# Performance work log

Hardware: AMD Instinct MI355X
Metric: run time of the kernel (lower is better)

The kernel has to match this reference:

```python
import jax, jax.numpy as jnp
import numpy as np

N = 8192        # nodes
E = 131072      # edges (avg degree 16)
IN_DIM = 6      # x_end - x_start
HID = 256
OUT = 256
N_EXP = 8
N_LAYERS = 3
TOP_K = 2
N_GRAPHS = 64


def setup_inputs() -> dict:
    key = jax.random.key(0)
    ks = jax.random.split(key, 12)
    def lin(k, fan_in, shape):
        return jax.random.normal(k, shape, jnp.float32) * (1.0 / np.sqrt(fan_in))
    x = jax.random.normal(ks[0], (N, IN_DIM), jnp.float32)
    edge_index = jax.random.randint(ks[1], (2, E), 0, N)
    batch = jnp.sort(jax.random.randint(ks[2], (N,), 0, N_GRAPHS))
    return {
        "x": x,
        "edge_index": edge_index,
        "batch": batch,
        "enc_W": lin(ks[3], IN_DIM, (IN_DIM, HID)),
        "enc_b": jnp.zeros((HID,), jnp.float32),
        "q_W": lin(ks[4], HID + 2, (HID + 2, HID)),
        "q_b": jnp.zeros((HID,), jnp.float32),
        "k_W": lin(ks[5], HID + 2, (HID + 2, HID)),
        "k_b": jnp.zeros((HID,), jnp.float32),
        "v_W": lin(ks[6], HID + 2, (HID + 2, HID)),
        "v_b": jnp.zeros((HID,), jnp.float32),
        "out_W": lin(ks[7], HID, (HID, N_EXP)),
        "out_b": jnp.zeros((N_EXP,), jnp.float32),
        "exp_Wh": lin(ks[8], HID, (N_EXP, N_LAYERS - 1, HID, HID)),
        "exp_bh": jnp.zeros((N_EXP, N_LAYERS - 1, HID), jnp.float32),
        "exp_Wo": lin(ks[9], HID, (N_EXP, HID, OUT)),
        "exp_bo": jnp.zeros((N_EXP, OUT), jnp.float32),
    }


def reference(x, edge_index, batch, enc_W, enc_b, q_W, q_b, k_W, k_b,
              v_W, v_b, out_W, out_b, exp_Wh, exp_bh, exp_Wo, exp_bo):
    # --- shared encoder ---
    h = jax.nn.relu(x @ enc_W + enc_b)                     # [N, HID]

    # --- per-graph size features broadcast back to nodes ---
    src, dst = edge_index[0], edge_index[1]
    ones_n = jnp.ones((N,), h.dtype)
    ones_e = jnp.ones((E,), h.dtype)
    nodes_per_g = jax.ops.segment_sum(ones_n, batch, num_segments=N_GRAPHS)
    edges_per_g = jax.ops.segment_sum(ones_e, batch[src], num_segments=N_GRAPHS)
    size_feat = jnp.stack([jnp.log1p(nodes_per_g)[batch],
                           jnp.log1p(edges_per_g)[batch]], axis=-1)  # [N, 2]

    z = jnp.concatenate([h, size_feat], axis=-1)           # [N, HID+2]

    # --- dense self-attention router ---
    q = z @ q_W + q_b
    k = z @ k_W + k_b
    v = z @ v_W + v_b
    scale = 1.0 / np.sqrt(z.shape[-1])
    attn = jax.nn.softmax((q @ k.T) * scale, axis=-1)      # [N, N]
    fused = attn @ v                                       # [N, HID]
    logits = fused @ out_W + out_b                         # [N, N_EXP]

    # --- sparse top-k routing (renormalized top-k of softmax probs) ---
    probs = jax.nn.softmax(logits, axis=-1)
    top_v, top_i = jax.lax.top_k(probs, TOP_K)
    rows = jnp.arange(N)[:, None]
    sparse = jnp.zeros_like(probs).at[rows, top_i].set(top_v)
    sparse = sparse / sparse.sum(axis=-1, keepdims=True)   # [N, N_EXP]

    # --- experts: stacked graph-conv towers (vectorized over experts) ---
    deg = jnp.clip(jax.ops.segment_sum(ones_e, dst, num_segments=N), 1.0, None)
    def neigh_mean(He):  # He: [N_EXP, N, d]
        agg = jax.vmap(lambda he: jax.ops.segment_sum(he[src], dst, num_segments=N))(He)
        return agg / deg[None, :, None]

    He = jnp.broadcast_to(h[None], (N_EXP, N, HID))
    for l in range(N_LAYERS - 1):
        He = jax.nn.relu(
            jnp.einsum('enh,ehk->enk', He + neigh_mean(He), exp_Wh[:, l])
            + exp_bh[:, l][:, None, :])
    Y = jnp.einsum('enh,eho->eno', He + neigh_mean(He), exp_Wo) + exp_bo[:, None, :]

    # --- top-k dense-masked combine: (y * sparse[...,None]).sum(expert dim) ---
    return jnp.einsum('eno,ne->no', Y, sparse)             # [N, OUT]
```

## Files before the change

### kernel.cpp

```cpp
#include <hip/hip_runtime.h>
#include <math.h>

#define NN 8192
#define NE 131072
#define ZK 288
#define NG 64
#define ASPLIT 16
#define QB 256
#define KB 32

typedef __attribute__((ext_vector_type(8))) short bf16x8;
typedef __attribute__((ext_vector_type(4))) float f32x4;
typedef __attribute__((ext_vector_type(8))) _Float16 f16x8;
typedef __attribute__((ext_vector_type(4))) _Float16 f16x4;

static __device__ __forceinline__ unsigned short f2bf(float f) {
    unsigned u = __float_as_uint(f);
    unsigned r = (u + 0x7FFFu + ((u >> 16) & 1u)) >> 16;
    return (unsigned short)r;
}
static __device__ __forceinline__ float b2f(unsigned short h) {
    return __uint_as_float(((unsigned)h) << 16);
}

__global__ __launch_bounds__(256) void k_counts(const int* __restrict__ ei,
    const int* __restrict__ batch, int* ncnt, int* ecnt, int* indeg)
{
    __shared__ int he[NG], hn[NG];
    const int t = threadIdx.x, b = blockIdx.x;
    if (t < NG) { he[t] = 0; hn[t] = 0; }
    __syncthreads();
    const int e0 = b * (NE / 64);
#pragma unroll
    for (int i = 0; i < (NE / 64) / 256; ++i) {
        int idx = e0 + i * 256 + t;
        int src = ei[idx], dst = ei[NE + idx];
        atomicAdd(&he[batch[src]], 1);
        atomicAdd(&indeg[dst], 1);
    }
    if (t < 128) atomicAdd(&hn[batch[b * 128 + t]], 1);
    __syncthreads();
    if (t < NG) {
        if (he[t]) atomicAdd(&ecnt[t], he[t]);
        if (hn[t]) atomicAdd(&ncnt[t], hn[t]);
    }
}

__global__ __launch_bounds__(256) void k_encoder(const float* __restrict__ x,
    const float* __restrict__ encW, const float* __restrict__ encb,
    const int* __restrict__ batch, const int* __restrict__ ncnt,
    const int* __restrict__ ecnt, float* __restrict__ z,
    unsigned short* __restrict__ zb)
{
    int n = blockIdx.x, c = threadIdx.x;
    __shared__ float xr[8];
    if (c < 6) xr[c] = x[n * 6 + c];
    __syncthreads();
    float a = encb[c];
#pragma unroll
    for (int i = 0; i < 6; ++i) a = fmaf(xr[i], encW[i * 256 + c], a);
    float h = fmaxf(a, 0.f);
    z[n * ZK + c] = h;
    zb[n * 256 + c] = f2bf(h);
    if (c == 0) {
        int g = batch[n];
        z[n * ZK + 256] = log1pf((float)ncnt[g]);
        z[n * ZK + 257] = log1pf((float)ecnt[g]);
    }
    if (c >= 2 && c < 32) z[n * ZK + 256 + c] = 0.f;
}

__global__ __launch_bounds__(256) void k_scan(const int* __restrict__ indeg,
                                              int* __restrict__ rowptr)
{
    __shared__ int part[256];
    int t = threadIdx.x;
    int base = t * 32, s = 0;
    for (int i = 0; i < 32; ++i) s += indeg[base + i];
    part[t] = s;
    __syncthreads();
    if (t == 0) {
        int run = 0;
        for (int i = 0; i < 256; ++i) { int v = part[i]; part[i] = run; run += v; }
        rowptr[NN] = run;
    }
    __syncthreads();
    int run = part[t];
    for (int i = 0; i < 32; ++i) { rowptr[base + i] = run; run += indeg[base + i]; }
}

__global__ __launch_bounds__(256) void k_fill(const int* __restrict__ ei,
    const int* __restrict__ rowptr, int* __restrict__ cursor, int* __restrict__ colidx)
{
    int tid = blockIdx.x * 256 + threadIdx.x;
    if (tid >= NE) return;
    int dst = ei[NE + tid];
    int pos = atomicAdd(&cursor[dst], 1);
    colidx[rowptr[dst] + pos] = ei[tid];
}

__global__ __launch_bounds__(256) void k_prep_qk(const float* __restrict__ qW,
    const float* __restrict__ kW, float* __restrict__ Wq, float* __restrict__ Wk)
{
    int idx = blockIdx.x * 256 + threadIdx.x;
    int r = idx >> 8, c = idx & 255;
    Wq[idx] = (r < 258) ? qW[r * 256 + c] : 0.f;
    Wk[idx] = (r < 258) ? kW[r * 256 + c] : 0.f;
}

__global__ __launch_bounds__(256) void k_prep_vo(const float* __restrict__ vW,
    const float* __restrict__ vb, const float* __restrict__ outW,
    float* __restrict__ Wvo, float* __restrict__ bvo)
{
    int idx = blockIdx.x * 256 + threadIdx.x;
    if (idx < ZK * 8) {
        int r = idx >> 3, e = idx & 7;
        float s = 0.f;
        if (r < 258)
            for (int c = 0; c < 256; ++c) s = fmaf(vW[r * 256 + c], outW[c * 8 + e], s);
        Wvo[idx] = s;
    } else if (idx < ZK * 8 + 8) {
        int e = idx - ZK * 8;
        float s = 0.f;
        for (int c = 0; c < 256; ++c) s = fmaf(vb[c], outW[c * 8 + e], s);
        bvo[e] = s;
    }
}

__global__ __launch_bounds__(256) void k_prep_w(const float* __restrict__ eWh,
    const float* __restrict__ eWo, unsigned short* __restrict__ Bth,
    unsigned short* __restrict__ Bto)
{
    int id = blockIdx.x * 256 + threadIdx.x;
    if (id < 16 * 65536) {
        int h = id & 255, kcol = (id >> 8) & 255, m = id >> 16;
        Bth[id] = f2bf(eWh[((size_t)m * 256 + h) * 256 + kcol]);
    } else if (id < 24 * 65536) {
        int j = id - 16 * 65536;
        int h = j & 255, o = (j >> 8) & 255, e = j >> 16;
        Bto[j] = f2bf(eWo[((size_t)e * 256 + h) * 256 + o]);
    }
}

__global__ __launch_bounds__(256) void k_gemm_qk(
    const float* __restrict__ A,
    const float* __restrict__ Wq, const float* __restrict__ Wk,
    const float* __restrict__ qb, const float* __restrict__ kb,
    _Float16* __restrict__ qh, _Float16* __restrict__ ql,
    _Float16* __restrict__ kh, _Float16* __restrict__ kl,
    float scale, int K)
{
    const float* B    = blockIdx.z ? Wk : Wq;
    const float* bias = blockIdx.z ? kb : qb;
    _Float16* Ch = blockIdx.z ? kh : qh;
    _Float16* Cl = blockIdx.z ? kl : ql;
    const float scl = blockIdx.z ? 1.0f : scale;
    __shared__ float As[32][132];
    __shared__ float Bs[32][68];
    int t = threadIdx.x;
    int m0 = blockIdx.y * 128, n0 = blockIdx.x * 64;
    int tr = t & 15, tc = t >> 4;
    float acc[8][4];
#pragma unroll
    for (int i = 0; i < 8; ++i)
#pragma unroll
        for (int j = 0; j < 4; ++j) acc[i][j] = 0.f;

    for (int k0 = 0; k0 < K; k0 += 32) {
#pragma unroll
        for (int i = 0; i < 4; ++i) {
            int f = t + 256 * i;
            int kc = f & 7, row = f >> 3;
            float4 v = *(const float4*)&A[(size_t)(m0 + row) * ZK + k0 + 4 * kc];
            As[4 * kc + 0][row] = v.x; As[4 * kc + 1][row] = v.y;
            As[4 * kc + 2][row] = v.z; As[4 * kc + 3][row] = v.w;
        }
#pragma unroll
        for (int i = 0; i < 2; ++i) {
            int f = t + 256 * i;
            int nc = f & 15, krow = f >> 4;
            *(float4*)&Bs[krow][4 * nc] =
                *(const float4*)&B[(size_t)(k0 + krow) * 256 + n0 + 4 * nc];
        }
        __syncthreads();
#pragma unroll
        for (int kk = 0; kk < 32; ++kk) {
            float4 a0 = *(const float4*)&As[kk][4 * tr];
            float4 a1 = *(const float4*)&As[kk][64 + 4 * tr];
            float4 b  = *(const float4*)&Bs[kk][4 * tc];
            const float av0[4] = {a0.x, a0.y, a0.z, a0.w};
            const float av1[4] = {a1.x, a1.y, a1.z, a1.w};
            const float bv[4]  = {b.x, b.y, b.z, b.w};
#pragma unroll
            for (int i = 0; i < 4; ++i)
#pragma unroll
                for (int j = 0; j < 4; ++j) {
                    acc[i][j]     = fmaf(av0[i], bv[j], acc[i][j]);
                    acc[4 + i][j] = fmaf(av1[i], bv[j], acc[4 + i][j]);
                }
        }
        __syncthreads();
    }
    float4 bi = *(const float4*)&bias[n0 + 4 * tc];
    const float bb[4] = {bi.x, bi.y, bi.z, bi.w};
#pragma unroll
    for (int h = 0; h < 2; ++h)
#pragma unroll
        for (int i = 0; i < 4; ++i) {
            int m = m0 + h * 64 + 4 * tr + i;
            f16x4 vh, vl;
#pragma unroll
            for (int j = 0; j < 4; ++j) {
                float v = (acc[h * 4 + i][j] + bb[j]) * scl;
                _Float16 hi = (_Float16)v;
                vh[j] = hi;
                vl[j] = (_Float16)(v - (float)hi);
            }
            *(f16x4*)&Ch[(size_t)m * 256 + n0 + 4 * tc] = vh;
            *(f16x4*)&Cl[(size_t)m * 256 + n0 + 4 * tc] = vl;
        }
}

__global__ __launch_bounds__(512) void k_gemm_bf(
    const unsigned short* __restrict__ A,
    const unsigned short* __restrict__ Bt,
    const float* __restrict__ bias,
    unsigned short* __restrict__ Cb,
    float* __restrict__ Ys,
    const float* __restrict__ sparse,
    const int* __restrict__ i1,
    long long aStrideZ, long long btStrideZ, long long cStrideZ, int biasStrideZ,
    int mode)
{
    const int bid = blockIdx.x;
    const int ez = bid & 7;
    const int tile = bid >> 3;
    const int n0 = (tile & 1) * 128, m0 = (tile >> 1) * 128;
    A    += (size_t)ez * aStrideZ;
    Bt   += (size_t)ez * btStrideZ;
    bias += (size_t)ez * biasStrideZ;
    if (mode == 0) Cb += (size_t)ez * cStrideZ;
    __shared__ unsigned short As[128][40];
    __shared__ unsigned short Bs[128][40];
    const int t = threadIdx.x;
    const int wid = t >> 6, lane = t & 63;
    const int wr = wid >> 2, wc = wid & 3;
    const int lr = lane & 15, lg = lane >> 4;
    f32x4 acc[4][2];
#pragma unroll
    for (int mf = 0; mf < 4; ++mf)
#pragma unroll
        for (int nf = 0; nf < 2; ++nf) acc[mf][nf] = (f32x4){0.f, 0.f, 0.f, 0.f};

    const int rA = t >> 2, cA = t & 3;
    for (int k0 = 0; k0 < 256; k0 += 32) {
        uint4 va = *(const uint4*)&A[(size_t)(m0 + rA) * 256 + k0 + 8 * cA];
        uint4 vB = *(const uint4*)&Bt[(size_t)(n0 + rA) * 256 + k0 + 8 * cA];
        *(uint4*)&As[rA][8 * cA] = va;
        *(uint4*)&Bs[rA][8 * cA] = vB;
        __syncthreads();
        bf16x8 a[4], b[2];
#pragma unroll
        for (int mf = 0; mf < 4; ++mf)
            a[mf] = *(const bf16x8*)&As[wr * 64 + mf * 16 + lr][8 * lg];
#pragma unroll
        for (int nf = 0; nf < 2; ++nf)
            b[nf] = *(const bf16x8*)&Bs[wc * 32 + nf * 16 + lr][8 * lg];
#pragma unroll
        for (int mf = 0; mf < 4; ++mf)
#pragma unroll
            for (int nf = 0; nf < 2; ++nf)
                acc[mf][nf] = __builtin_amdgcn_mfma_f32_16x16x32_bf16(
                    a[mf], b[nf], acc[mf][nf], 0, 0, 0);
        __syncthreads();
    }
    if (mode == 0) {
#pragma unroll
        for (int mf = 0; mf < 4; ++mf)
#pragma unroll
            for (int reg = 0; reg < 4; ++reg) {
                int m = m0 + wr * 64 + mf * 16 + lg * 4 + reg;
#pragma unroll
                for (int nf = 0; nf < 2; ++nf) {
                    int c = n0 + wc * 32 + nf * 16 + lr;
                    float v = acc[mf][nf][reg] + bias[c];
                    Cb[(size_t)m * 256 + c] = f2bf(fmaxf(v, 0.f));
                }
            }
    } else {
#pragma unroll
        for (int mf = 0; mf < 4; ++mf)
#pragma unroll
            for (int reg = 0; reg < 4; ++reg) {
                int m = m0 + wr * 64 + mf * 16 + lg * 4 + reg;
                float w = sparse[m * 8 + ez];
                if (w != 0.f) {
                    int slot = (ez == i1[m]) ? 0 : 1;
                    float* dst = Ys + (size_t)slot * NN * 256 + (size_t)m * 256;
#pragma unroll
                    for (int nf = 0; nf < 2; ++nf) {
                        int c = n0 + wc * 32 + nf * 16 + lr;
                        dst[c] = w * (acc[mf][nf][reg] + bias[c]);
                    }
                }
            }
    }
}

__global__ __launch_bounds__(256) void k_vo(const float* __restrict__ z,
    const float* __restrict__ Wvo, const float* __restrict__ bvo,
    float* __restrict__ vo)
{
    int n = blockIdx.x * 4 + (threadIdx.x >> 6);
    int lane = threadIdx.x & 63;
    float p[8];
#pragma unroll
    for (int e = 0; e < 8; ++e) p[e] = 0.f;
    for (int kk = lane; kk < ZK; kk += 64) {
        float zv = z[(size_t)n * ZK + kk];
        float4 w0 = *(const float4*)&Wvo[kk * 8];
        float4 w1 = *(const float4*)&Wvo[kk * 8 + 4];
        p[0] = fmaf(zv, w0.x, p[0]); p[1] = fmaf(zv, w0.y, p[1]);
        p[2] = fmaf(zv, w0.z, p[2]); p[3] = fmaf(zv, w0.w, p[3]);
        p[4] = fmaf(zv, w1.x, p[4]); p[5] = fmaf(zv, w1.y, p[5]);
        p[6] = fmaf(zv, w1.z, p[6]); p[7] = fmaf(zv, w1.w, p[7]);
    }
#pragma unroll
    for (int msk = 1; msk <= 32; msk <<= 1)
#pragma unroll
        for (int e = 0; e < 8; ++e) p[e] += __shfl_xor(p[e], msk);
    if (lane == 0) {
#pragma unroll
        for (int e = 0; e < 8; ++e) vo[n * 8 + e] = p[e] + bvo[e];
    }
}

__global__ __launch_bounds__(512, 2) void k_attn_mfma(
    const _Float16* __restrict__ qh_, const _Float16* __restrict__ ql_,
    const _Float16* __restrict__ kh, const _Float16* __restrict__ kl,
    const float* __restrict__ vo, float* __restrict__ pm,
    float* __restrict__ pl, float* __restrict__ pacc)
{
    __shared__ uint4 lds[2][KB * 64];
    const int bid = blockIdx.x;
    const int split = bid & 15;
    const int rowblk = bid >> 4;
    const int n0 = rowblk * QB;
    const int t = threadIdx.x, w = t >> 6, lane = t & 63;
    const int g = lane >> 4, c = lane & 15;

    f16x8 bqh[2][8], bql[2][8];
#pragma unroll
    for (int rs = 0; rs < 2; ++rs) {
        const int row = n0 + w * 32 + rs * 16 + c;
#pragma unroll
        for (int st = 0; st < 8; ++st) {
            bqh[rs][st] = *(const f16x8*)&qh_[(size_t)row * 256 + st * 32 + g * 8];
            bql[rs][st] = *(const f16x8*)&ql_[(size_t)row * 256 + st * 32 + g * 8];
        }
    }
    float m_[2] = {-INFINITY, -INFINITY};
    float l_[2] = {0.f, 0.f};
    float pv[2][8];
#pragma unroll
    for (int rs = 0; rs < 2; ++rs)
#pragma unroll
        for (int e = 0; e < 8; ++e) pv[rs][e] = 0.f;

    const int kbase0 = split * (NN / ASPLIT);
    auto STAGE = [&](int buf, int kb) {
#pragma unroll
        for (int i = 0; i < 4; ++i) {
            int u = i * 512 + t;
            int key = u >> 6;
            int half = (u >> 5) & 1;
            int c16 = (u & 31) ^ (key & 7);
            const _Float16* src = half ? kl : kh;
            const _Float16* gp = src + (size_t)(kb + key) * 256 + c16 * 8;
            uint4* lp = &lds[buf][i * 512 + (t & ~63)];
            __builtin_amdgcn_global_load_lds(
                (const __attribute__((address_space(1))) void*)gp,
                (__attribute__((address_space(3))) void*)lp, 16, 0, 0);
        }
    };
    STAGE(0, kbase0);
    __syncthreads();
    int cur = 0;
    const int NCH = (NN / ASPLIT) / KB;
    for (int ch = 0; ch < NCH; ++ch) {
        const int kbase = kbase0 + ch * KB;
        if (ch + 1 < NCH) STAGE(cur ^ 1, kbase + KB);
#pragma unroll
        for (int kt = 0; kt < 2; ++kt) {
            const char* kbp = (const char*)lds[cur] + (kt * 16 + c) * 1024;
            const int swz = ((kt * 16 + c) & 7) << 4;
            f32x4 acc0 = (f32x4){0.f, 0.f, 0.f, 0.f};
            f32x4 acc1 = (f32x4){0.f, 0.f, 0.f, 0.f};
#pragma unroll
            for (int st = 0; st < 8; ++st) {
                const int off = (st * 64 + g * 16) ^ swz;
                f16x8 kah = *(const f16x8*)(kbp + off);
                f16x8 kal = *(const f16x8*)(kbp + 512 + off);
                acc0 = __builtin_amdgcn_mfma_f32_16x16x32_f16(kah, bqh[0][st], acc0, 0, 0, 0);
                acc0 = __builtin_amdgcn_mfma_f32_16x16x32_f16(kal, bqh[0][st], acc0, 0, 0, 0);
                acc0 = __builtin_amdgcn_mfma_f32_16x16x32_f16(kah, bql[0][st], acc0, 0, 0, 0);
                acc1 = __builtin_amdgcn_mfma_f32_16x16x32_f16(kah, bqh[1][st], acc1, 0, 0, 0);
                acc1 = __builtin_amdgcn_mfma_f32_16x16x32_f16(kal, bqh[1][st], acc1, 0, 0, 0);
                acc1 = __builtin_amdgcn_mfma_f32_16x16x32_f16(kah, bql[1][st], acc1, 0, 0, 0);
            }
            const int kb2 = kbase + kt * 16 + 4 * g;
            float4 w0[4], w1[4];
#pragma unroll
            for (int r = 0; r < 4; ++r) {
                w0[r] = *(const float4*)&vo[(kb2 + r) * 8];
                w1[r] = *(const float4*)&vo[(kb2 + r) * 8 + 4];
            }
#pragma unroll
            for (int rs = 0; rs < 2; ++rs) {
                f32x4 s = rs ? acc1 : acc0;
                float cm = fmaxf(fmaxf(s[0], s[1]), fmaxf(s[2], s[3]));
                float mn = fmaxf(m_[rs], cm);
                float rsc = __expf(m_[rs] - mn);
                float p0 = __expf(s[0] - mn);
                float p1 = __expf(s[1] - mn);
                float p2 = __expf(s[2] - mn);
                float p3 = __expf(s[3] - mn);
                l_[rs] = l_[rs] * rsc + (p0 + p1 + p2 + p3);
                m_[rs] = mn;
                pv[rs][0] = pv[rs][0]*rsc + p0*w0[0].x + p1*w0[1].x + p2*w0[2].x + p3*w0[3].x;
                pv[rs][1] = pv[rs][1]*rsc + p0*w0[0].y + p1*w0[1].y + p2*w0[2].y + p3*w0[3].y;
                pv[rs][2] = pv[rs][2]*rsc + p0*w0[0].z + p1*w0[1].z + p2*w0[2].z + p3*w0[3].z;
                pv[rs][3] = pv[rs][3]*rsc + p0*w0[0].w + p1*w0[1].w + p2*w0[2].w + p3*w0[3].w;
                pv[rs][4] = pv[rs][4]*rsc + p0*w1[0].x + p1*w1[1].x + p2*w1[2].x + p3*w1[3].x;
                pv[rs][5] = pv[rs][5]*rsc + p0*w1[0].y + p1*w1[1].y + p2*w1[2].y + p3*w1[3].y;
                pv[rs][6] = pv[rs][6]*rsc + p0*w1[0].z + p1*w1[1].z + p2*w1[2].z + p3*w1[3].z;
                pv[rs][7] = pv[rs][7]*rsc + p0*w1[0].w + p1*w1[1].w + p2*w1[2].w + p3*w1[3].w;
            }
        }
        __syncthreads();
        cur ^= 1;
    }
#pragma unroll
    for (int msk = 16; msk <= 32; msk <<= 1) {
#pragma unroll
        for (int rs = 0; rs < 2; ++rs) {
            float mo = __shfl_xor(m_[rs], msk);
            float lo = __shfl_xor(l_[rs], msk);
            float mn = fmaxf(m_[rs], mo);
            float a = __expf(m_[rs] - mn), b = __expf(mo - mn);
            l_[rs] = l_[rs] * a + lo * b;
#pragma unroll
            for (int e = 0; e < 8; ++e) {
                float po = __shfl_xor(pv[rs][e], msk);
                pv[rs][e] = pv[rs][e] * a + po * b;
            }
            m_[rs] = mn;
        }
    }
    if (g == 0) {
#pragma unroll
        for (int rs = 0; rs < 2; ++rs) {
            int n = n0 + w * 32 + rs * 16 + c;
            pm[split * NN + n] = m_[rs];
            pl[split * NN + n] = l_[rs];
#pragma unroll
            for (int e = 0; e < 8; ++e)
                pacc[(size_t)split * NN * 8 + n * 8 + e] = pv[rs][e];
        }
    }
}

__global__ __launch_bounds__(256) void k_attn_merge(
    const float* __restrict__ pm, const float* __restrict__ pl,
    const float* __restrict__ pacc, const float* __restrict__ outb,
    float* __restrict__ sparse, int* __restrict__ i1o)
{
    int n = blockIdx.x * 256 + threadIdx.x;
    float mn = -INFINITY;
#pragma unroll
    for (int s = 0; s < ASPLIT; ++s) mn = fmaxf(mn, pm[s * NN + n]);
    float l = 0.f;
    float lg[8];
#pragma unroll
    for (int e = 0; e < 8; ++e) lg[e] = 0.f;
#pragma unroll
    for (int s = 0; s < ASPLIT; ++s) {
        float r = __expf(pm[s * NN + n] - mn);
        l += pl[s * NN + n] * r;
#pragma unroll
        for (int e = 0; e < 8; ++e)
            lg[e] += pacc[(size_t)s * NN * 8 + n * 8 + e] * r;
    }
    float inv = 1.f / l;
#pragma unroll
    for (int e = 0; e < 8; ++e) lg[e] = lg[e] * inv + outb[e];
    int i1 = 0; float v1 = lg[0];
#pragma unroll
    for (int e = 1; e < 8; ++e) if (lg[e] > v1) { v1 = lg[e]; i1 = e; }
    int i2 = -1; float v2 = -INFINITY;
#pragma unroll
    for (int e = 0; e < 8; ++e) if (e != i1 && lg[e] > v2) { v2 = lg[e]; i2 = e; }
    float e2 = __expf(v2 - v1);
    float w1 = 1.f / (1.f + e2);
    float w2 = e2 / (1.f + e2);
#pragma unroll
    for (int e = 0; e < 8; ++e)
        sparse[n * 8 + e] = (e == i1) ? w1 : ((e == i2) ? w2 : 0.f);
    i1o[n] = i1;
}

__global__ __launch_bounds__(256) void k_agg_b2b(
    const unsigned short* __restrict__ HeAll, const int* __restrict__ rowptr,
    const int* __restrict__ colidx, unsigned short* __restrict__ XAll,
    int eshift)
{
    const int bid = blockIdx.x;
    const int e = bid & ((1 << eshift) - 1);
    const int nb = bid >> eshift;
    const unsigned short* He = HeAll + (size_t)e * NN * 256;
    unsigned short* X = XAll + (size_t)e * NN * 256;
    int n = nb * 4 + (threadIdx.x >> 6);
    int c4 = (threadIdx.x & 63) * 4;
    int r0 = rowptr[n], r1 = rowptr[n + 1];
    float a0 = 0.f, a1 = 0.f, a2 = 0.f, a3 = 0.f;
    float b0 = 0.f, b1 = 0.f, b2 = 0.f, b3 = 0.f;
    float e0 = 0.f, e1 = 0.f, e2 = 0.f, e3 = 0.f;
    float d0 = 0.f, d1 = 0.f, d2 = 0.f, d3 = 0.f;
    int i = r0;
    for (; i + 4 <= r1; i += 4) {
        int s0 = colidx[i], s1 = colidx[i + 1], s2 = colidx[i + 2], s3 = colidx[i + 3];
        ushort4 v0 = *(const ushort4*)&He[(size_t)s0 * 256 + c4];
        ushort4 v1 = *(const ushort4*)&He[(size_t)s1 * 256 + c4];
        ushort4 v2 = *(const ushort4*)&He[(size_t)s2 * 256 + c4];
        ushort4 v3 = *(const ushort4*)&He[(size_t)s3 * 256 + c4];
        a0 += b2f(v0.x); a1 += b2f(v0.y); a2 += b2f(v0.z); a3 += b2f(v0.w);
        b0 += b2f(v1.x); b1 += b2f(v1.y); b2 += b2f(v1.z); b3 += b2f(v1.w);
        e0 += b2f(v2.x); e1 += b2f(v2.y); e2 += b2f(v2.z); e3 += b2f(v2.w);
        d0 += b2f(v3.x); d1 += b2f(v3.y); d2 += b2f(v3.z); d3 += b2f(v3.w);
    }
    for (; i < r1; ++i) {
        int sn = colidx[i];
        ushort4 v = *(const ushort4*)&He[(size_t)sn * 256 + c4];
        a0 += b2f(v.x); a1 += b2f(v.y); a2 += b2f(v.z); a3 += b2f(v.w);
    }
    a0 += b0 + e0 + d0; a1 += b1 + e1 + d1;
    a2 += b2 + e2 + d2; a3 += b3 + e3 + d3;
    int deg = r1 - r0;
    float inv = 1.f / (float)(deg > 1 ? deg : 1);
    ushort4 self = *(const ushort4*)&He[(size_t)n * 256 + c4];
    ushort4 o;
    o.x = f2bf(b2f(self.x) + a0 * inv); o.y = f2bf(b2f(self.y) + a1 * inv);
    o.z = f2bf(b2f(self.z) + a2 * inv); o.w = f2bf(b2f(self.w) + a3 * inv);
    *(ushort4*)&X[(size_t)n * 256 + c4] = o;
}

__global__ __launch_bounds__(256) void k_combine2(const float* __restrict__ Ys,
                                                  float* __restrict__ out)
{
    int i = (blockIdx.x * 256 + threadIdx.x) * 4;
    float4 a = *(const float4*)&Ys[i];
    float4 b = *(const float4*)&Ys[(size_t)NN * 256 + i];
    float4 o;
    o.x = a.x + b.x; o.y = a.y + b.y; o.z = a.z + b.z; o.w = a.w + b.w;
    *(float4*)&out[i] = o;
}

extern "C" void kernel_launch(void* const* d_in, const int* in_sizes, int n_in,
                              void* d_out, int out_size, void* d_ws, size_t ws_size,
                              hipStream_t stream)
{
    (void)n_in; (void)out_size;
    const float* x     = (const float*)d_in[0];
    const int*   ei    = (const int*)d_in[1];
    const int*   batch = (const int*)d_in[2];
    const float* encW  = (const float*)d_in[3];
    const float* encb  = (const float*)d_in[4];
    const float* qW    = (const float*)d_in[5];
    const float* qb    = (const float*)d_in[6];
    const float* kW    = (const float*)d_in[7];
    const float* kb    = (const float*)d_in[8];
    const float* vW    = (const float*)d_in[9];
    const float* vb    = (const float*)d_in[10];
    const float* outW  = (const float*)d_in[11];
    const float* outb  = (const float*)d_in[12];
    const float* eWh   = (const float*)d_in[13];
    const float* ebh   = (const float*)d_in[14];
    const float* eWo   = (const float*)d_in[15];
    const float* ebo   = (const float*)d_in[16];
    float* out = (float*)d_out;
    if (in_sizes[0] != NN * 6 || in_sizes[1] != 2 * NE) return;

    char* wsp = (char*)d_ws;
    size_t off = 0;
    auto alloc = [&](size_t bytes) -> void* {
        void* p = wsp + off;
        off += (bytes + 511) & ~(size_t)511;
        return p;
    };
    float* z   = (float*)alloc((size_t)NN * ZK * 4);
    unsigned short* zb = (unsigned short*)alloc((size_t)NN * 256 * 2);
    _Float16* qh = (_Float16*)alloc((size_t)4 * NN * 256 * 2);
    _Float16* ql = qh + (size_t)NN * 256;
    _Float16* kh = ql + (size_t)NN * 256;
    _Float16* kl = kh + (size_t)NN * 256;
    float* Ys = (float*)qh;
    float* vo     = (float*)alloc((size_t)NN * 8 * 4);
    float* sparse = (float*)alloc((size_t)NN * 8 * 4);
    int*   i1buf  = (int*)alloc((size_t)NN * 4);
    unsigned short* Xball = (unsigned short*)alloc((size_t)8 * NN * 256 * 2);
    unsigned short* Heb   = (unsigned short*)alloc((size_t)8 * NN * 256 * 2);
    unsigned short* Bth   = (unsigned short*)alloc((size_t)16 * 65536 * 2);
    unsigned short* Bto   = (unsigned short*)alloc((size_t)8 * 65536 * 2);
    float* Wq   = (float*)alloc((size_t)ZK * 256 * 4);
    float* Wk   = (float*)alloc((size_t)ZK * 256 * 4);
    float* Wvo  = (float*)alloc((size_t)ZK * 8 * 4);
    float* bvo  = (float*)alloc(8 * 4);
    float* pm   = (float*)alloc((size_t)ASPLIT * NN * 4);
    float* plb  = (float*)alloc((size_t)ASPLIT * NN * 4);
    float* pacc = (float*)alloc((size_t)ASPLIT * NN * 8 * 4);
    int* ints   = (int*)alloc((size_t)(NG + NG + NN + NN) * 4);
    int* ncnt = ints, *ecnt = ints + NG, *indeg = ecnt + NG, *cursor = indeg + NN;
    int* rowptr = (int*)alloc((size_t)(NN + 1) * 4);
    int* colidx = (int*)alloc((size_t)NE * 4);
    if (off > ws_size) return;

    hipMemsetAsync(ints, 0, (size_t)(NG + NG + NN + NN) * 4, stream);
    k_counts<<<64, 256, 0, stream>>>(ei, batch, ncnt, ecnt, indeg);
    k_prep_qk<<<ZK, 256, 0, stream>>>(qW, kW, Wq, Wk);
    k_prep_vo<<<(ZK * 8 + 8 + 255) / 256, 256, 0, stream>>>(vW, vb, outW, Wvo, bvo);
    k_prep_w<<<(24 * 65536) / 256, 256, 0, stream>>>(eWh, eWo, Bth, Bto);
    k_encoder<<<NN, 256, 0, stream>>>(x, encW, encb, batch, ncnt, ecnt, z, zb);
    k_scan<<<1, 256, 0, stream>>>(indeg, rowptr);
    k_fill<<<(NE + 255) / 256, 256, 0, stream>>>(ei, rowptr, cursor, colidx);

    float scale = 1.f / sqrtf(258.f);
    dim3 gqk(256 / 64, NN / 128, 2);
    k_gemm_qk<<<gqk, 256, 0, stream>>>(z, Wq, Wk, qb, kb, qh, ql, kh, kl, scale, ZK);
    k_vo<<<NN / 4, 256, 0, stream>>>(z, Wvo, bvo, vo);

    k_attn_mfma<<<(NN / QB) * ASPLIT, 512, 0, stream>>>(qh, ql, kh, kl, vo, pm, plb, pacc);
    k_attn_merge<<<NN / 256, 256, 0, stream>>>(pm, plb, pacc, outb, sparse, i1buf);

    k_agg_b2b<<<NN / 4, 256, 0, stream>>>(zb, rowptr, colidx, Xball, 0);
    k_gemm_bf<<<1024, 512, 0, stream>>>(Xball, Bth, ebh, Heb, nullptr, nullptr, nullptr,
                                        0, (long long)2 * 65536, (long long)NN * 256,
                                        2 * 256, 0);
    k_agg_b2b<<<(NN / 4) * 8, 256, 0, stream>>>(Heb, rowptr, colidx, Xball, 3);
    k_gemm_bf<<<1024, 512, 0, stream>>>(Xball, Bth + 65536, ebh + 256, Heb,
                                        nullptr, nullptr, nullptr,
                                        (long long)NN * 256, (long long)2 * 65536,
                                        (long long)NN * 256, 2 * 256, 0);
    k_agg_b2b<<<(NN / 4) * 8, 256, 0, stream>>>(Heb, rowptr, colidx, Xball, 3);
    k_gemm_bf<<<1024, 512, 0, stream>>>(Xball, Bto, ebo, nullptr, Ys, sparse, i1buf,
                                        (long long)NN * 256, (long long)65536,
                                        0, 256, 1);
    k_combine2<<<(NN * 256 / 4) / 256, 256, 0, stream>>>(Ys, out);
}
```

Baseline: 398.3 us.

## Compact final expert layer to routed rows only and prioritize attention MFMA

Result: slower. 410.7 us (+3.1%).

```diff
diff --git a/kernel.cpp b/kernel.cpp
--- a/kernel.cpp
+++ b/kernel.cpp
@@ -229,6 +229,8 @@
     float* __restrict__ Ys,
     const float* __restrict__ sparse,
     const int* __restrict__ i1,
+    const int* __restrict__ rowlist,
+    const int* __restrict__ rcnt,
     long long aStrideZ, long long btStrideZ, long long cStrideZ, int biasStrideZ,
     int mode)
 {
@@ -236,6 +238,8 @@
     const int ez = bid & 7;
     const int tile = bid >> 3;
     const int n0 = (tile & 1) * 128, m0 = (tile >> 1) * 128;
+    const int cnt = (mode == 1) ? rcnt[ez] : 0;
+    if (mode == 1 && m0 >= cnt) return;
     A    += (size_t)ez * aStrideZ;
     Bt   += (size_t)ez * btStrideZ;
     bias += (size_t)ez * biasStrideZ;
@@ -293,14 +297,17 @@
 #pragma unroll
             for (int reg = 0; reg < 4; ++reg) {
                 int m = m0 + wr * 64 + mf * 16 + lg * 4 + reg;
-                float w = sparse[m * 8 + ez];
-                if (w != 0.f) {
-                    int slot = (ez == i1[m]) ? 0 : 1;
-                    float* dst = Ys + (size_t)slot * NN * 256 + (size_t)m * 256;
-#pragma unroll
-                    for (int nf = 0; nf < 2; ++nf) {
-                        int c = n0 + wc * 32 + nf * 16 + lr;
-                        dst[c] = w * (acc[mf][nf][reg] + bias[c]);
+                if (m < cnt) {
+                    int n = rowlist[ez * NN + m];
+                    float w = sparse[n * 8 + ez];
+                    if (w != 0.f) {
+                        int slot = (ez == i1[n]) ? 0 : 1;
+                        float* dst = Ys + (size_t)slot * NN * 256 + (size_t)n * 256;
+#pragma unroll
+                        for (int nf = 0; nf < 2; ++nf) {
+                            int c = n0 + wc * 32 + nf * 16 + lr;
+                            dst[c] = w * (acc[mf][nf][reg] + bias[c]);
+                        }
                     }
                 }
             }
@@ -396,6 +403,7 @@
             const int swz = ((kt * 16 + c) & 7) << 4;
             f32x4 acc0 = (f32x4){0.f, 0.f, 0.f, 0.f};
             f32x4 acc1 = (f32x4){0.f, 0.f, 0.f, 0.f};
+            __builtin_amdgcn_s_setprio(1);
 #pragma unroll
             for (int st = 0; st < 8; ++st) {
                 const int off = (st * 64 + g * 16) ^ swz;
@@ -408,6 +416,7 @@
                 acc1 = __builtin_amdgcn_mfma_f32_16x16x32_f16(kal, bqh[1][st], acc1, 0, 0, 0);
                 acc1 = __builtin_amdgcn_mfma_f32_16x16x32_f16(kah, bql[1][st], acc1, 0, 0, 0);
             }
+            __builtin_amdgcn_s_setprio(0);
             const int kb2 = kbase + kt * 16 + 4 * g;
             float4 w0[4], w1[4];
 #pragma unroll
@@ -507,6 +516,31 @@
     for (int e = 0; e < 8; ++e)
         sparse[n * 8 + e] = (e == i1) ? w1 : ((e == i2) ? w2 : 0.f);
     i1o[n] = i1;
+}
+
+__global__ __launch_bounds__(256) void k_rows(const float* __restrict__ sparse,
+    int* __restrict__ rcnt, int* __restrict__ rowlist)
+{
+    __shared__ int lcnt[8], lbase[8];
+    const int t = threadIdx.x;
+    const int n = blockIdx.x * 256 + t;
+    if (t < 8) lcnt[t] = 0;
+    __syncthreads();
+    int myexp[2], myslot[2];
+    int cnt = 0;
+#pragma unroll
+    for (int e = 0; e < 8; ++e) {
+        if (sparse[n * 8 + e] != 0.f && cnt < 2) {
+            myexp[cnt] = e;
+            myslot[cnt] = atomicAdd(&lcnt[e], 1);
+            ++cnt;
+        }
+    }
+    __syncthreads();
+    if (t < 8) lbase[t] = atomicAdd(&rcnt[t], lcnt[t]);
+    __syncthreads();
+    for (int j = 0; j < cnt; ++j)
+        rowlist[myexp[j] * NN + lbase[myexp[j]] + myslot[j]] = n;
 }
 
 __global__ __launch_bounds__(256) void k_agg_b2b(
@@ -554,6 +588,55 @@
     *(ushort4*)&X[(size_t)n * 256 + c4] = o;
 }
 
+__global__ __launch_bounds__(256) void k_agg_rows(
+    const unsigned short* __restrict__ HeAll, const int* __restrict__ rowptr,
+    const int* __restrict__ colidx, const int* __restrict__ rowlist,
+    const int* __restrict__ rcnt, unsigned short* __restrict__ XAll)
+{
+    const int bid = blockIdx.x;
+    const int e = bid & 7;
+    const int nb = bid >> 3;
+    const int cnt = rcnt[e];
+    const int r = nb * 4 + (threadIdx.x >> 6);
+    if (nb * 4 >= cnt) return;
+    if (r >= cnt) return;
+    const unsigned short* He = HeAll + (size_t)e * NN * 256;
+    unsigned short* X = XAll + (size_t)e * NN * 256;
+    const int n = rowlist[e * NN + r];
+    int c4 = (threadIdx.x & 63) * 4;
+    int r0 = rowptr[n], r1 = rowptr[n + 1];
+    float a0 = 0.f, a1 = 0.f, a2 = 0.f, a3 = 0.f;
+    float b0 = 0.f, b1 = 0.f, b2 = 0.f, b3 = 0.f;
+    float e0 = 0.f, e1 = 0.f, e2 = 0.f, e3 = 0.f;
+    float d0 = 0.f, d1 = 0.f, d2 = 0.f, d3 = 0.f;
+    int i = r0;
+    for (; i + 4 <= r1; i += 4) {
+        int s0 = colidx[i], s1 = colidx[i + 1], s2 = colidx[i + 2], s3 = colidx[i + 3];
+        ushort4 v0 = *(const ushort4*)&He[(size_t)s0 * 256 + c4];
+        ushort4 v1 = *(const ushort4*)&He[(size_t)s1 * 256 + c4];
+        ushort4 v2 = *(const ushort4*)&He[(size_t)s2 * 256 + c4];
+        ushort4 v3 = *(const ushort4*)&He[(size_t)s3 * 256 + c4];
+        a0 += b2f(v0.x); a1 += b2f(v0.y); a2 += b2f(v0.z); a3 += b2f(v0.w);
+        b0 += b2f(v1.x); b1 += b2f(v1.y); b2 += b2f(v1.z); b3 += b2f(v1.w);
+        e0 += b2f(v2.x); e1 += b2f(v2.y); e2 += b2f(v2.z); e3 += b2f(v2.w);
+        d0 += b2f(v3.x); d1 += b2f(v3.y); d2 += b2f(v3.z); d3 += b2f(v3.w);
+    }
+    for (; i < r1; ++i) {
+        int sn = colidx[i];
+        ushort4 v = *(const ushort4*)&He[(size_t)sn * 256 + c4];
+        a0 += b2f(v.x); a1 += b2f(v.y); a2 += b2f(v.z); a3 += b2f(v.w);
+    }
+    a0 += b0 + e0 + d0; a1 += b1 + e1 + d1;
+    a2 += b2 + e2 + d2; a3 += b3 + e3 + d3;
+    int deg = r1 - r0;
+    float inv = 1.f / (float)(deg > 1 ? deg : 1);
+    ushort4 self = *(const ushort4*)&He[(size_t)n * 256 + c4];
+    ushort4 o;
+    o.x = f2bf(b2f(self.x) + a0 * inv); o.y = f2bf(b2f(self.y) + a1 * inv);
+    o.z = f2bf(b2f(self.z) + a2 * inv); o.w = f2bf(b2f(self.w) + a3 * inv);
+    *(ushort4*)&X[(size_t)r * 256 + c4] = o;
+}
+
 __global__ __launch_bounds__(256) void k_combine2(const float* __restrict__ Ys,
                                                   float* __restrict__ out)
 {
@@ -607,6 +690,7 @@
     float* vo     = (float*)alloc((size_t)NN * 8 * 4);
     float* sparse = (float*)alloc((size_t)NN * 8 * 4);
     int*   i1buf  = (int*)alloc((size_t)NN * 4);
+    int*   rowlist = (int*)alloc((size_t)8 * NN * 4);
     unsigned short* Xball = (unsigned short*)alloc((size_t)8 * NN * 256 * 2);
     unsigned short* Heb   = (unsigned short*)alloc((size_t)8 * NN * 256 * 2);
     unsigned short* Bth   = (unsigned short*)alloc((size_t)16 * 65536 * 2);
@@ -618,13 +702,14 @@
     float* pm   = (float*)alloc((size_t)ASPLIT * NN * 4);
     float* plb  = (float*)alloc((size_t)ASPLIT * NN * 4);
     float* pacc = (float*)alloc((size_t)ASPLIT * NN * 8 * 4);
-    int* ints   = (int*)alloc((size_t)(NG + NG + NN + NN) * 4);
+    int* ints   = (int*)alloc((size_t)(NG + NG + NN + NN + 8) * 4);
     int* ncnt = ints, *ecnt = ints + NG, *indeg = ecnt + NG, *cursor = indeg + NN;
+    int* rcnt = cursor + NN;
     int* rowptr = (int*)alloc((size_t)(NN + 1) * 4);
     int* colidx = (int*)alloc((size_t)NE * 4);
     if (off > ws_size) return;
 
-    hipMemsetAsync(ints, 0, (size_t)(NG + NG + NN + NN) * 4, stream);
+    hipMemsetAsync(ints, 0, (size_t)(NG + NG + NN + NN + 8) * 4, stream);
     k_counts<<<64, 256, 0, stream>>>(ei, batch, ncnt, ecnt, indeg);
     k_prep_qk<<<ZK, 256, 0, stream>>>(qW, kW, Wq, Wk);
     k_prep_vo<<<(ZK * 8 + 8 + 255) / 256, 256, 0, stream>>>(vW, vb, outW, Wvo, bvo);
@@ -640,18 +725,21 @@
 
     k_attn_mfma<<<(NN / QB) * ASPLIT, 512, 0, stream>>>(qh, ql, kh, kl, vo, pm, plb, pacc);
     k_attn_merge<<<NN / 256, 256, 0, stream>>>(pm, plb, pacc, outb, sparse, i1buf);
+    k_rows<<<NN / 256, 256, 0, stream>>>(sparse, rcnt, rowlist);
 
     k_agg_b2b<<<NN / 4, 256, 0, stream>>>(zb, rowptr, colidx, Xball, 0);
-    k_gemm_bf<<<1024, 512, 0, stream>>>(Xball, Bth, ebh, Heb, nullptr, nullptr, nullptr,
+    k_gemm_bf<<<1024, 512, 0, stream>>>(Xball, Bth, ebh, Heb, nullptr, nullptr,
+                                        nullptr, nullptr, nullptr,
                                         0, (long long)2 * 65536, (long long)NN * 256,
                                         2 * 256, 0);
     k_agg_b2b<<<(NN / 4) * 8, 256, 0, stream>>>(Heb, rowptr, colidx, Xball, 3);
     k_gemm_bf<<<1024, 512, 0, stream>>>(Xball, Bth + 65536, ebh + 256, Heb,
-                                        nullptr, nullptr, nullptr,
+                                        nullptr, nullptr, nullptr, nullptr, nullptr,
                                         (long long)NN * 256, (long long)2 * 65536,
                                         (long long)NN * 256, 2 * 256, 0);
-    k_agg_b2b<<<(NN / 4) * 8, 256, 0, stream>>>(Heb, rowptr, colidx, Xball, 3);
+    k_agg_rows<<<(NN / 4) * 8, 256, 0, stream>>>(Heb, rowptr, colidx, rowlist, rcnt, Xball);
     k_gemm_bf<<<1024, 512, 0, stream>>>(Xball, Bto, ebo, nullptr, Ys, sparse, i1buf,
+                                        rowlist, rcnt,
                                         (long long)NN * 256, (long long)65536,
                                         0, 256, 1);
     k_combine2<<<(NN * 256 / 4) / 256, 256, 0, stream>>>(Ys, out);
```

## Move Q/K projection GEMM to split-fp16 MFMA and raise attention MFMA priority

Applied to the files above, without the earlier changes.

Result: faster. 384.5 us (median of 2 runs) (-3.4%).

```diff
diff --git a/kernel.cpp b/kernel.cpp
--- a/kernel.cpp
+++ b/kernel.cpp
@@ -49,8 +49,8 @@
 __global__ __launch_bounds__(256) void k_encoder(const float* __restrict__ x,
     const float* __restrict__ encW, const float* __restrict__ encb,
     const int* __restrict__ batch, const int* __restrict__ ncnt,
-    const int* __restrict__ ecnt, float* __restrict__ z,
-    unsigned short* __restrict__ zb)
+    const int* __restrict__ ecnt, _Float16* __restrict__ zh,
+    _Float16* __restrict__ zl, unsigned short* __restrict__ zb)
 {
     int n = blockIdx.x, c = threadIdx.x;
     __shared__ float xr[8];
@@ -60,14 +60,24 @@
 #pragma unroll
     for (int i = 0; i < 6; ++i) a = fmaf(xr[i], encW[i * 256 + c], a);
     float h = fmaxf(a, 0.f);
-    z[n * ZK + c] = h;
+    _Float16 hi = (_Float16)h;
+    zh[(size_t)n * ZK + c] = hi;
+    zl[(size_t)n * ZK + c] = (_Float16)(h - (float)hi);
     zb[n * 256 + c] = f2bf(h);
     if (c == 0) {
         int g = batch[n];
-        z[n * ZK + 256] = log1pf((float)ncnt[g]);
-        z[n * ZK + 257] = log1pf((float)ecnt[g]);
-    }
-    if (c >= 2 && c < 32) z[n * ZK + 256 + c] = 0.f;
+        float s0 = log1pf((float)ncnt[g]);
+        float s1 = log1pf((float)ecnt[g]);
+        _Float16 h0 = (_Float16)s0, h1 = (_Float16)s1;
+        zh[(size_t)n * ZK + 256] = h0;
+        zl[(size_t)n * ZK + 256] = (_Float16)(s0 - (float)h0);
+        zh[(size_t)n * ZK + 257] = h1;
+        zl[(size_t)n * ZK + 257] = (_Float16)(s1 - (float)h1);
+    }
+    if (c >= 2 && c < 32) {
+        zh[(size_t)n * ZK + 256 + c] = (_Float16)0.f;
+        zl[(size_t)n * ZK + 256 + c] = (_Float16)0.f;
+    }
 }
 
 __global__ __launch_bounds__(256) void k_scan(const int* __restrict__ indeg,
@@ -99,13 +109,19 @@
     colidx[rowptr[dst] + pos] = ei[tid];
 }
 
-__global__ __launch_bounds__(256) void k_prep_qk(const float* __restrict__ qW,
-    const float* __restrict__ kW, float* __restrict__ Wq, float* __restrict__ Wk)
+__global__ __launch_bounds__(256) void k_prep_qkw(const float* __restrict__ qW,
+    const float* __restrict__ kW, _Float16* __restrict__ Wth,
+    _Float16* __restrict__ Wtl)
 {
     int idx = blockIdx.x * 256 + threadIdx.x;
-    int r = idx >> 8, c = idx & 255;
-    Wq[idx] = (r < 258) ? qW[r * 256 + c] : 0.f;
-    Wk[idx] = (r < 258) ? kW[r * 256 + c] : 0.f;
+    int r = idx % ZK;
+    int c = (idx / ZK) & 255;
+    int sel = idx / (ZK * 256);
+    const float* W = sel ? kW : qW;
+    float w = (r < 258) ? W[r * 256 + c] : 0.f;
+    _Float16 hi = (_Float16)w;
+    Wth[idx] = hi;
+    Wtl[idx] = (_Float16)(w - (float)hi);
 }
 
 __global__ __launch_bounds__(256) void k_prep_vo(const float* __restrict__ vW,
@@ -142,82 +158,76 @@
     }
 }
 
-__global__ __launch_bounds__(256) void k_gemm_qk(
-    const float* __restrict__ A,
-    const float* __restrict__ Wq, const float* __restrict__ Wk,
+__global__ __launch_bounds__(512) void k_gemm_qk(
+    const _Float16* __restrict__ zh, const _Float16* __restrict__ zl,
+    const _Float16* __restrict__ Wth, const _Float16* __restrict__ Wtl,
     const float* __restrict__ qb, const float* __restrict__ kb,
-    _Float16* __restrict__ qh, _Float16* __restrict__ ql,
-    _Float16* __restrict__ kh, _Float16* __restrict__ kl,
-    float scale, int K)
-{
-    const float* B    = blockIdx.z ? Wk : Wq;
-    const float* bias = blockIdx.z ? kb : qb;
-    _Float16* Ch = blockIdx.z ? kh : qh;
-    _Float16* Cl = blockIdx.z ? kl : ql;
-    const float scl = blockIdx.z ? 1.0f : scale;
-    __shared__ float As[32][132];
-    __shared__ float Bs[32][68];
-    int t = threadIdx.x;
-    int m0 = blockIdx.y * 128, n0 = blockIdx.x * 64;
-    int tr = t & 15, tc = t >> 4;
-    float acc[8][4];
-#pragma unroll
-    for (int i = 0; i < 8; ++i)
-#pragma unroll
-        for (int j = 0; j < 4; ++j) acc[i][j] = 0.f;
-
-    for (int k0 = 0; k0 < K; k0 += 32) {
-#pragma unroll
-        for (int i = 0; i < 4; ++i) {
-            int f = t + 256 * i;
-            int kc = f & 7, row = f >> 3;
-            float4 v = *(const float4*)&A[(size_t)(m0 + row) * ZK + k0 + 4 * kc];
-            As[4 * kc + 0][row] = v.x; As[4 * kc + 1][row] = v.y;
-            As[4 * kc + 2][row] = v.z; As[4 * kc + 3][row] = v.w;
-        }
-#pragma unroll
-        for (int i = 0; i < 2; ++i) {
-            int f = t + 256 * i;
-            int nc = f & 15, krow = f >> 4;
-            *(float4*)&Bs[krow][4 * nc] =
-                *(const float4*)&B[(size_t)(k0 + krow) * 256 + n0 + 4 * nc];
-        }
+    _Float16* __restrict__ qho, _Float16* __restrict__ qlo,
+    _Float16* __restrict__ kho, _Float16* __restrict__ klo, float scale)
+{
+    const int bid = blockIdx.x;
+    const int sel = bid & 1;
+    const int tile = bid >> 1;
+    const int n0 = (tile & 1) * 128, m0 = (tile >> 1) * 128;
+    const _Float16* Bh = Wth + (size_t)sel * 256 * ZK;
+    const _Float16* Bl = Wtl + (size_t)sel * 256 * ZK;
+    const float* bias = sel ? kb : qb;
+    _Float16* Ch = sel ? kho : qho;
+    _Float16* Cl = sel ? klo : qlo;
+    const float scl = sel ? 1.0f : scale;
+    __shared__ _Float16 Ash[128][40], Asl[128][40];
+    __shared__ _Float16 Bsh[128][40], Bsl[128][40];
+    const int t = threadIdx.x;
+    const int wid = t >> 6, lane = t & 63;
+    const int wr = wid >> 2, wc = wid & 3;
+    const int lr = lane & 15, lg = lane >> 4;
+    f32x4 acc[4][2];
+#pragma unroll
+    for (int mf = 0; mf < 4; ++mf)
+#pragma unroll
+        for (int nf = 0; nf < 2; ++nf) acc[mf][nf] = (f32x4){0.f, 0.f, 0.f, 0.f};
+
+    const int rA = t >> 2, cA = t & 3;
+    for (int k0 = 0; k0 < ZK; k0 += 32) {
+        *(uint4*)&Ash[rA][8 * cA] = *(const uint4*)&zh[(size_t)(m0 + rA) * ZK + k0 + 8 * cA];
+        *(uint4*)&Asl[rA][8 * cA] = *(const uint4*)&zl[(size_t)(m0 + rA) * ZK + k0 + 8 * cA];
+        *(uint4*)&Bsh[rA][8 * cA] = *(const uint4*)&Bh[(size_t)(n0 + rA) * ZK + k0 + 8 * cA];
+        *(uint4*)&Bsl[rA][8 * cA] = *(const uint4*)&Bl[(size_t)(n0 + rA) * ZK + k0 + 8 * cA];
         __syncthreads();
-#pragma unroll
-        for (int kk = 0; kk < 32; ++kk) {
-            float4 a0 = *(const float4*)&As[kk][4 * tr];
-            float4 a1 = *(const float4*)&As[kk][64 + 4 * tr];
-            float4 b  = *(const float4*)&Bs[kk][4 * tc];
-            const float av0[4] = {a0.x, a0.y, a0.z, a0.w};
-            const float av1[4] = {a1.x, a1.y, a1.z, a1.w};
-            const float bv[4]  = {b.x, b.y, b.z, b.w};
-#pragma unroll
-            for (int i = 0; i < 4; ++i)
-#pragma unroll
-                for (int j = 0; j < 4; ++j) {
-                    acc[i][j]     = fmaf(av0[i], bv[j], acc[i][j]);
-                    acc[4 + i][j] = fmaf(av1[i], bv[j], acc[4 + i][j]);
-                }
-        }
+        f16x8 ah[4], al[4], bh[2], bl[2];
+#pragma unroll
+        for (int mf = 0; mf < 4; ++mf) {
+            ah[mf] = *(const f16x8*)&Ash[wr * 64 + mf * 16 + lr][8 * lg];
+            al[mf] = *(const f16x8*)&Asl[wr * 64 + mf * 16 + lr][8 * lg];
+        }
+#pragma unroll
+        for (int nf = 0; nf < 2; ++nf) {
+            bh[nf] = *(const f16x8*)&Bsh[wc * 32 + nf * 16 + lr][8 * lg];
+            bl[nf] = *(const f16x8*)&Bsl[wc * 32 + nf * 16 + lr][8 * lg];
+        }
+#pragma unroll
+        for (int mf = 0; mf < 4; ++mf)
+#pragma unroll
+            for (int nf = 0; nf < 2; ++nf) {
+                acc[mf][nf] = __builtin_amdgcn_mfma_f32_16x16x32_f16(ah[mf], bh[nf], acc[mf][nf], 0, 0, 0);
+                acc[mf][nf] = __builtin_amdgcn_mfma_f32_16x16x32_f16(ah[mf], bl[nf], acc[mf][nf], 0, 0, 0);
+                acc[mf][nf] = __builtin_amdgcn_mfma_f32_16x16x32_f16(al[mf], bh[nf], acc[mf][nf], 0, 0, 0);
+            }
         __syncthreads();
     }
-    float4 bi = *(const float4*)&bias[n0 + 4 * tc];
-    const float bb[4] = {bi.x, bi.y, bi.z, bi.w};
-#pragma unroll
-    for (int h = 0; h < 2; ++h)
-#pragma unroll
-        for (int i = 0; i < 4; ++i) {
-            int m = m0 + h * 64 + 4 * tr + i;
-            f16x4 vh, vl;
-#pragma unroll
-            for (int j = 0; j < 4; ++j) {
-                float v = (acc[h * 4 + i][j] + bb[j]) * scl;
+#pragma unroll
+    for (int mf = 0; mf < 4; ++mf)
+#pragma unroll
+        for (int reg = 0; reg < 4; ++reg) {
+            int m = m0 + wr * 64 + mf * 16 + lg * 4 + reg;
+#pragma unroll
+            for (int nf = 0; nf < 2; ++nf) {
+                int c = n0 + wc * 32 + nf * 16 + lr;
+                float v = (acc[mf][nf][reg] + bias[c]) * scl;
                 _Float16 hi = (_Float16)v;
-                vh[j] = hi;
-                vl[j] = (_Float16)(v - (float)hi);
-            }
-            *(f16x4*)&Ch[(size_t)m * 256 + n0 + 4 * tc] = vh;
-            *(f16x4*)&Cl[(size_t)m * 256 + n0 + 4 * tc] = vl;
+                Ch[(size_t)m * 256 + c] = hi;
+                Cl[(size_t)m * 256 + c] = (_Float16)(v - (float)hi);
+            }
         }
 }
 
@@ -307,9 +317,9 @@
     }
 }
 
-__global__ __launch_bounds__(256) void k_vo(const float* __restrict__ z,
-    const float* __restrict__ Wvo, const float* __restrict__ bvo,
-    float* __restrict__ vo)
+__global__ __launch_bounds__(256) void k_vo(const _Float16* __restrict__ zh,
+    const _Float16* __restrict__ zl, const float* __restrict__ Wvo,
+    const float* __restrict__ bvo, float* __restrict__ vo)
 {
     int n = blockIdx.x * 4 + (threadIdx.x >> 6);
     int lane = threadIdx.x & 63;
@@ -317,7 +327,7 @@
 #pragma unroll
     for (int e = 0; e < 8; ++e) p[e] = 0.f;
     for (int kk = lane; kk < ZK; kk += 64) {
-        float zv = z[(size_t)n * ZK + kk];
+        float zv = (float)zh[(size_t)n * ZK + kk] + (float)zl[(size_t)n * ZK + kk];
         float4 w0 = *(const float4*)&Wvo[kk * 8];
         float4 w1 = *(const float4*)&Wvo[kk * 8 + 4];
         p[0] = fmaf(zv, w0.x, p[0]); p[1] = fmaf(zv, w0.y, p[1]);
@@ -396,6 +406,7 @@
             const int swz = ((kt * 16 + c) & 7) << 4;
             f32x4 acc0 = (f32x4){0.f, 0.f, 0.f, 0.f};
             f32x4 acc1 = (f32x4){0.f, 0.f, 0.f, 0.f};
+            __builtin_amdgcn_s_setprio(1);
 #pragma unroll
             for (int st = 0; st < 8; ++st) {
                 const int off = (st * 64 + g * 16) ^ swz;
@@ -408,6 +419,7 @@
                 acc1 = __builtin_amdgcn_mfma_f32_16x16x32_f16(kal, bqh[1][st], acc1, 0, 0, 0);
                 acc1 = __builtin_amdgcn_mfma_f32_16x16x32_f16(kah, bql[1][st], acc1, 0, 0, 0);
             }
+            __builtin_amdgcn_s_setprio(0);
             const int kb2 = kbase + kt * 16 + 4 * g;
             float4 w0[4], w1[4];
 #pragma unroll
@@ -597,7 +609,8 @@
         off += (bytes + 511) & ~(size_t)511;
         return p;
     };
-    float* z   = (float*)alloc((size_t)NN * ZK * 4);
+    _Float16* zh = (_Float16*)alloc((size_t)NN * ZK * 2);
+    _Float16* zl = (_Float16*)alloc((size_t)NN * ZK * 2);
     unsigned short* zb = (unsigned short*)alloc((size_t)NN * 256 * 2);
     _Float16* qh = (_Float16*)alloc((size_t)4 * NN * 256 * 2);
     _Float16* ql = qh + (size_t)NN * 256;
@@ -611,8 +624,8 @@
     unsigned short* Heb   = (unsigned short*)alloc((size_t)8 * NN * 256 * 2);
     unsigned short* Bth   = (unsigned short*)alloc((size_t)16 * 65536 * 2);
     unsigned short* Bto   = (unsigned short*)alloc((size_t)8 * 65536 * 2);
-    float* Wq   = (float*)alloc((size_t)ZK * 256 * 4);
-    float* Wk   = (float*)alloc((size_t)ZK * 256 * 4);
+    _Float16* Wth = (_Float16*)alloc((size_t)2 * 256 * ZK * 2);
+    _Float16* Wtl = (_Float16*)alloc((size_t)2 * 256 * ZK * 2);
     float* Wvo  = (float*)alloc((size_t)ZK * 8 * 4);
     float* bvo  = (float*)alloc(8 * 4);
     float* pm   = (float*)alloc((size_t)ASPLIT * NN * 4);
@@ -626,17 +639,17 @@
 
     hipMemsetAsync(ints, 0, (size_t)(NG + NG + NN + NN) * 4, stream);
     k_counts<<<64, 256, 0, stream>>>(ei, batch, ncnt, ecnt, indeg);
-    k_prep_qk<<<ZK, 256, 0, stream>>>(qW, kW, Wq, Wk);
+    k_prep_qkw<<<(2 * 256 * ZK) / 256, 256, 0, stream>>>(qW, kW, Wth, Wtl);
     k_prep_vo<<<(ZK * 8 + 8 + 255) / 256, 256, 0, stream>>>(vW, vb, outW, Wvo, bvo);
     k_prep_w<<<(24 * 65536) / 256, 256, 0, stream>>>(eWh, eWo, Bth, Bto);
-    k_encoder<<<NN, 256, 0, stream>>>(x, encW, encb, batch, ncnt, ecnt, z, zb);
+    k_encoder<<<NN, 256, 0, stream>>>(x, encW, encb, batch, ncnt, ecnt, zh, zl, zb);
     k_scan<<<1, 256, 0, stream>>>(indeg, rowptr);
     k_fill<<<(NE + 255) / 256, 256, 0, stream>>>(ei, rowptr, cursor, colidx);
 
     float scale = 1.f / sqrtf(258.f);
-    dim3 gqk(256 / 64, NN / 128, 2);
-    k_gemm_qk<<<gqk, 256, 0, stream>>>(z, Wq, Wk, qb, kb, qh, ql, kh, kl, scale, ZK);
-    k_vo<<<NN / 4, 256, 0, stream>>>(z, Wvo, bvo, vo);
+    k_gemm_qk<<<256, 512, 0, stream>>>(zh, zl, Wth, Wtl, qb, kb,
+                                       qh, ql, kh, kl, scale);
+    k_vo<<<NN / 4, 256, 0, stream>>>(zh, zl, Wvo, bvo, vo);
 
     k_attn_mfma<<<(NN / QB) * ASPLIT, 512, 0, stream>>>(qh, ql, kh, kl, vo, pm, plb, pacc);
     k_attn_merge<<<NN / 256, 256, 0, stream>>>(pm, plb, pacc, outb, sparse, i1buf);
```
